# Kernel tuning notes

Hardware: AMD Instinct MI355X
Metric: run time of the kernel (lower is better)

## Reference

```python
import jax, jax.numpy as jnp
import numpy as np

# shapes
B, S, D, V = 2, 2048, 1024, 32000
C = 8            # n_cycles
P = 256          # actual planes = min(n_planes_init, D // 2)
EPS = 1.1920929e-07  # torch RMSNorm default eps for float32 (finfo.eps)


def _rmsnorm(x, w):
    ms = jnp.mean(x * x, axis=-1, keepdims=True)
    return x * jax.lax.rsqrt(ms + EPS) * w


def setup_inputs() -> dict:
    key = jax.random.key(0)
    ks = jax.random.split(key, 10)
    tokens = jax.random.randint(ks[0], (B, S), 0, V, dtype=jnp.int32)
    embed_weight = jax.random.normal(ks[1], (V, D), dtype=jnp.float32) * 0.02
    lm_head_weight = jax.random.normal(ks[2], (V, D), dtype=jnp.float32) * 0.02
    out_norm_weight = jnp.ones((D,), dtype=jnp.float32)
    # per-cycle learned params (non-trivial values for numerics)
    angles = jax.random.normal(ks[3], (C, P), dtype=jnp.float32) * 0.1
    scales = 1.0 + jax.random.normal(ks[4], (C, D), dtype=jnp.float32) * 0.01
    shifts = jax.random.normal(ks[5], (C, D), dtype=jnp.float32) * 0.01
    norm_weights = 1.0 + jax.random.normal(ks[6], (C, D), dtype=jnp.float32) * 0.01
    mix_weight = jnp.array([0.1, 0.8, 0.1], dtype=jnp.float32)
    # plane pairs: per-cycle permutation of D, pi = perm[:P], pj = perm[P:2P]
    pi_list, pj_list = [], []
    for c in range(C):
        perm = jax.random.permutation(jax.random.fold_in(ks[7], c), D)
        pi_list.append(perm[:P])
        pj_list.append(perm[P:2 * P])
    pi_all = jnp.stack(pi_list).astype(jnp.int32)  # [C, P]
    pj_all = jnp.stack(pj_list).astype(jnp.int32)  # [C, P]
    return {
        "tokens": tokens,
        "embed_weight": embed_weight,
        "angles": angles,
        "scales": scales,
        "shifts": shifts,
        "norm_weights": norm_weights,
        "mix_weight": mix_weight,
        "out_norm_weight": out_norm_weight,
        "lm_head_weight": lm_head_weight,
        "pi_all": pi_all,
        "pj_all": pj_all,
    }


def reference(tokens, embed_weight, angles, scales, shifts, norm_weights,
              mix_weight, out_norm_weight, lm_head_weight, pi_all, pj_all):
    x = embed_weight[tokens].astype(jnp.float32)  # [B, S, D]
    n_cycles = angles.shape[0]
    for c in range(n_cycles):
        # temporal mix: shifted-left / self / shifted-right
        left = jnp.pad(x[:, :-1, :], ((0, 0), (1, 0), (0, 0)))
        right = jnp.pad(x[:, 1:, :], ((0, 0), (0, 1), (0, 0)))
        x = mix_weight[0] * left + mix_weight[1] * x + mix_weight[2] * right
        # Givens rotations on disjoint plane pairs (gather -> rotate -> scatter)
        pi, pj = pi_all[c], pj_all[c]
        cos_a = jnp.cos(angles[c])
        sin_a = jnp.sin(angles[c])
        xi = x[..., pi]  # [B, S, P]
        xj = x[..., pj]
        x_new = x.at[..., pi].set(xi * cos_a - xj * sin_a)
        x_new = x_new.at[..., pj].set(xi * sin_a + xj * cos_a)
        # scale/shift + SiLU, then RMSNorm residual update
        x_act = jax.nn.silu(x_new * scales[c] + shifts[c])
        x = x + _rmsnorm(x_act - x, norm_weights[c])
    x = _rmsnorm(x, out_norm_weight)
    return jnp.einsum("bsd,vd->bsv", x, lm_head_weight)  # [B, S, V]
```

## Files before the change

### kernel.cpp

```cpp
#include <hip/hip_runtime.h>

#define B_SZ   2
#define S_LEN  2048
#define D_DIM  1024
#define V_DIM  32000
#define NTOK   (B_SZ * S_LEN)
#define NCYC   8
#define NPLANES 256
#define EPS_F  1.1920929e-07f

typedef float  f32x4  __attribute__((ext_vector_type(4)));
typedef __bf16 bf16x8 __attribute__((ext_vector_type(8)));

__device__ __forceinline__ unsigned short f32_to_bf16(float f) {
    unsigned int u = __builtin_bit_cast(unsigned int, f);
    u += 0x7fffu + ((u >> 16) & 1u);
    return (unsigned short)(u >> 16);
}

__device__ __forceinline__ float block_reduce_sum(float v, float* red) {
    const int tid = threadIdx.x;
    #pragma unroll
    for (int off = 32; off > 0; off >>= 1) v += __shfl_down(v, off, 64);
    if ((tid & 63) == 0) red[tid >> 6] = v;
    __syncthreads();
    return red[0] + red[1] + red[2] + red[3];
}

__global__ __launch_bounds__(256) void k_embed(const int* __restrict__ tokens,
                                               const float* __restrict__ table,
                                               float* __restrict__ x) {
    const int t = blockIdx.x;
    const int tok = tokens[t];
    const float4* src = (const float4*)(table + (size_t)tok * D_DIM);
    float4* dst = (float4*)(x + (size_t)t * D_DIM);
    dst[threadIdx.x] = src[threadIdx.x];
}

__global__ __launch_bounds__(256) void k_cycle(
    const float* __restrict__ xin, float* __restrict__ xout,
    const float* __restrict__ angles, const float* __restrict__ scales,
    const float* __restrict__ shifts, const float* __restrict__ normw,
    const float* __restrict__ mixw, const int* __restrict__ pi,
    const int* __restrict__ pj)
{
    __shared__ float lx[D_DIM];
    __shared__ float red[4];
    const int t = blockIdx.x;
    const int s = t & (S_LEN - 1);
    const int tid = threadIdx.x;
    const int d0 = tid * 4;

    float4 sv = ((const float4*)(xin + (size_t)t * D_DIM))[tid];
    float4 lv = make_float4(0.f, 0.f, 0.f, 0.f);
    float4 rv = make_float4(0.f, 0.f, 0.f, 0.f);
    if (s > 0)         lv = ((const float4*)(xin + (size_t)(t - 1) * D_DIM))[tid];
    if (s < S_LEN - 1) rv = ((const float4*)(xin + (size_t)(t + 1) * D_DIM))[tid];
    const float mw0 = mixw[0], mw1 = mixw[1], mw2 = mixw[2];

    const float m0 = mw0 * lv.x + mw1 * sv.x + mw2 * rv.x;
    const float m1 = mw0 * lv.y + mw1 * sv.y + mw2 * rv.y;
    const float m2 = mw0 * lv.z + mw1 * sv.z + mw2 * rv.z;
    const float m3 = mw0 * lv.w + mw1 * sv.w + mw2 * rv.w;
    lx[d0 + 0] = m0; lx[d0 + 1] = m1; lx[d0 + 2] = m2; lx[d0 + 3] = m3;
    __syncthreads();

    const int ip = pi[tid], jp = pj[tid];
    float sa, ca;
    sincosf(angles[tid], &sa, &ca);
    const float xi = lx[ip], xj = lx[jp];
    __syncthreads();
    lx[ip] = xi * ca - xj * sa;
    lx[jp] = xi * sa + xj * ca;
    __syncthreads();

    const float4 sc = ((const float4*)scales)[tid];
    const float4 sh = ((const float4*)shifts)[tid];
    const float4 nw = ((const float4*)normw)[tid];
    const float xn0 = lx[d0 + 0], xn1 = lx[d0 + 1], xn2 = lx[d0 + 2], xn3 = lx[d0 + 3];
    const float a0 = xn0 * sc.x + sh.x;
    const float a1 = xn1 * sc.y + sh.y;
    const float a2 = xn2 * sc.z + sh.z;
    const float a3 = xn3 * sc.w + sh.w;
    const float r0 = a0 / (1.f + expf(-a0)) - m0;
    const float r1 = a1 / (1.f + expf(-a1)) - m1;
    const float r2 = a2 / (1.f + expf(-a2)) - m2;
    const float r3 = a3 / (1.f + expf(-a3)) - m3;

    const float tot = block_reduce_sum(r0 * r0 + r1 * r1 + r2 * r2 + r3 * r3, red);
    const float inv = rsqrtf(tot * (1.0f / D_DIM) + EPS_F);

    float4 o;
    o.x = m0 + r0 * inv * nw.x;
    o.y = m1 + r1 * inv * nw.y;
    o.z = m2 + r2 * inv * nw.z;
    o.w = m3 + r3 * inv * nw.w;
    ((float4*)(xout + (size_t)t * D_DIM))[tid] = o;
}

__global__ __launch_bounds__(256) void k_final(const float* __restrict__ xin,
                                               const float* __restrict__ ow,
                                               unsigned short* __restrict__ xb)
{
    __shared__ float red[4];
    const int t = blockIdx.x, tid = threadIdx.x;
    const float4 v = ((const float4*)(xin + (size_t)t * D_DIM))[tid];
    const float tot = block_reduce_sum(v.x * v.x + v.y * v.y + v.z * v.z + v.w * v.w, red);
    const float inv = rsqrtf(tot * (1.0f / D_DIM) + EPS_F);
    const float4 w = ((const float4*)ow)[tid];
    ushort4 o = make_ushort4(f32_to_bf16(v.x * inv * w.x),
                             f32_to_bf16(v.y * inv * w.y),
                             f32_to_bf16(v.z * inv * w.z),
                             f32_to_bf16(v.w * inv * w.w));
    ((ushort4*)xb)[(size_t)t * 256 + tid] = o;
}

__global__ __launch_bounds__(256) void k_cvt(const float* __restrict__ w,
                                             unsigned short* __restrict__ wb, int n4)
{
    int i = blockIdx.x * 256 + threadIdx.x;
    const int stride = gridDim.x * 256;
    for (; i < n4; i += stride) {
        const float4 v = ((const float4*)w)[i];
        ushort4 o = make_ushort4(f32_to_bf16(v.x), f32_to_bf16(v.y),
                                 f32_to_bf16(v.z), f32_to_bf16(v.w));
        ((ushort4*)wb)[i] = o;
    }
}

#define GLD_LDS(g, l)                                                          \
    __builtin_amdgcn_global_load_lds(                                          \
        (const __attribute__((address_space(1))) void*)(g),                    \
        (__attribute__((address_space(3))) void*)(l), 16, 0, 0)

#define STAGE_A(BUF, H, KT) do {                                               \
    GLD_LDS(gA + (size_t)(H) * 131072 + (size_t)(KT) * 64,                     \
            &lds[(BUF) * 32768 + (H) * 8192 + wave * 1024]);                   \
    GLD_LDS(gA + (size_t)(H) * 131072 + 8192 + (size_t)(KT) * 64,              \
            &lds[(BUF) * 32768 + (H) * 8192 + wave * 1024 + 512]);             \
} while (0)

#define STAGE_B(BUF, H, KT) do {                                               \
    GLD_LDS(gB + (size_t)(H) * 131072 + (size_t)(KT) * 64,                     \
            &lds[16384 + (BUF) * 32768 + (H) * 8192 + wave * 1024]);           \
    GLD_LDS(gB + (size_t)(H) * 131072 + 8192 + (size_t)(KT) * 64,              \
            &lds[16384 + (BUF) * 32768 + (H) * 8192 + wave * 1024 + 512]);     \
} while (0)

#define RD_A(BUF, MIB) do { _Pragma("unroll")                                  \
    for (int q_ = 0; q_ < 4; ++q_) {                                           \
        afr[q_][0] = *(const bf16x8*)&lds[(BUF) * 32768 + aoff + ((MIB) + q_) * 1024 + kx0]; \
        afr[q_][1] = *(const bf16x8*)&lds[(BUF) * 32768 + aoff + ((MIB) + q_) * 1024 + kx1]; \
    } } while (0)

#define RD_B(BUF, NIB, DST) do { _Pragma("unroll")                             \
    for (int n_ = 0; n_ < 2; ++n_) {                                           \
        DST[n_][0] = *(const bf16x8*)&lds[(BUF) * 32768 + boff + ((NIB) + n_) * 1024 + kx0]; \
        DST[n_][1] = *(const bf16x8*)&lds[(BUF) * 32768 + boff + ((NIB) + n_) * 1024 + kx1]; \
    } } while (0)

#define MFMA16(MIB, NIB, BF) do {                                              \
    __builtin_amdgcn_s_setprio(1);                                             \
    _Pragma("unroll") for (int m_ = 0; m_ < 4; ++m_)                           \
    _Pragma("unroll") for (int n_ = 0; n_ < 2; ++n_) {                         \
        acc[(MIB) + m_][(NIB) + n_] = __builtin_amdgcn_mfma_f32_16x16x32_bf16( \
            afr[m_][0], BF[n_][0], acc[(MIB) + m_][(NIB) + n_], 0, 0, 0);      \
        acc[(MIB) + m_][(NIB) + n_] = __builtin_amdgcn_mfma_f32_16x16x32_bf16( \
            afr[m_][1], BF[n_][1], acc[(MIB) + m_][(NIB) + n_], 0, 0, 0);      \
    }                                                                          \
    __builtin_amdgcn_s_setprio(0); } while (0)

#define PH_SYNC() do { __builtin_amdgcn_s_barrier();                           \
    asm volatile("s_waitcnt lgkmcnt(0)" ::: "memory"); } while (0)
#define PH_END() do { asm volatile("" ::: "memory");                           \
    __builtin_amdgcn_s_barrier(); } while (0)
#define VMCNT4() asm volatile("s_waitcnt vmcnt(4)" ::: "memory")

__global__ __launch_bounds__(512, 2) void k_gemm(
    const unsigned short* __restrict__ A,
    const unsigned short* __restrict__ Bw,
    float* __restrict__ C)
{
    __shared__ __align__(16) unsigned short lds[65536];
    const int tid = threadIdx.x;
    const int wave = tid >> 6, lane = tid & 63;
    const int wm = wave >> 2, wn = wave & 3;
    const int lr = lane & 15, kg = lane >> 4;

    const int swz = (blockIdx.x & 7) * 250 + (blockIdx.x >> 3);
    const int bm = swz / 125, bn = swz % 125;

    const int xr  = (lane & 7) * 8;
    const int kx0 = (kg * 8) ^ xr;
    const int kx1 = (32 + kg * 8) ^ xr;
    const int aoff = (wm * 128 + lr) * 64;
    const int boff = 16384 + (wn * 64 + lr) * 64;

    const int srow = lane >> 3;
    const int scol = ((lane & 7) ^ srow) * 8;
    const unsigned short* gA = A  + (size_t)(bm * 256 + wave * 16 + srow) * 1024 + scol;
    const unsigned short* gB = Bw + (size_t)(bn * 256 + wave * 16 + srow) * 1024 + scol;

    f32x4 acc[8][4];
    #pragma unroll
    for (int i = 0; i < 8; ++i)
        #pragma unroll
        for (int j = 0; j < 4; ++j) acc[i][j] = (f32x4){0.f, 0.f, 0.f, 0.f};
    bf16x8 afr[4][2], b01[2][2], b23[2][2];

    STAGE_A(0, 0, 0); STAGE_A(0, 1, 0);
    STAGE_B(0, 0, 0); STAGE_B(0, 1, 0);
    STAGE_B(1, 0, 1); STAGE_B(1, 1, 1);
    VMCNT4();
    __builtin_amdgcn_s_barrier();

    for (int j = 0; j < 8; ++j) {
        const int k1 = (2 * j + 1) & 15;
        const int k2 = (2 * j + 2) & 15;
        const int k3 = (2 * j + 3) & 15;
        RD_A(0, 0); RD_B(0, 0, b01);
        STAGE_A(1, 0, k1);
        PH_SYNC(); MFMA16(0, 0, b01); PH_END();

        RD_B(0, 2, b23);
        STAGE_A(1, 1, k1);
        PH_SYNC(); MFMA16(0, 2, b23); PH_END();

        RD_A(0, 4);
        STAGE_B(0, 0, k2);
        PH_SYNC(); MFMA16(4, 2, b23); PH_END();

        STAGE_B(0, 1, k2);
        VMCNT4();
        PH_SYNC(); MFMA16(4, 0, b01); PH_END();
        RD_A(1, 0); RD_B(1, 0, b01);
        STAGE_A(0, 0, k2);
        PH_SYNC(); MFMA16(0, 0, b01); PH_END();

        RD_B(1, 2, b23);
        STAGE_A(0, 1, k2);
        PH_SYNC(); MFMA16(0, 2, b23); PH_END();

        RD_A(1, 4);
        STAGE_B(1, 0, k3);
        PH_SYNC(); MFMA16(4, 2, b23); PH_END();

        STAGE_B(1, 1, k3);
        VMCNT4();
        PH_SYNC(); MFMA16(4, 0, b01); PH_END();
    }

    #pragma unroll
    for (int mi = 0; mi < 8; ++mi) {
        const size_t m0 = (size_t)(bm * 256 + wm * 128 + mi * 16 + kg * 4);
        #pragma unroll
        for (int ni = 0; ni < 4; ++ni) {
            const int n = bn * 256 + wn * 64 + ni * 16 + lr;
            float* cp = C + m0 * V_DIM + n;
            cp[0]                 = acc[mi][ni][0];
            cp[(size_t)V_DIM]     = acc[mi][ni][1];
            cp[(size_t)2 * V_DIM] = acc[mi][ni][2];
            cp[(size_t)3 * V_DIM] = acc[mi][ni][3];
        }
    }
}

extern "C" void kernel_launch(void* const* d_in, const int* in_sizes, int n_in,
                              void* d_out, int out_size, void* d_ws, size_t ws_size,
                              hipStream_t stream)
{
    const int*   tokens = (const int*)  d_in[0];
    const float* embedw = (const float*)d_in[1];
    const float* angles = (const float*)d_in[2];
    const float* scales = (const float*)d_in[3];
    const float* shifts = (const float*)d_in[4];
    const float* normw  = (const float*)d_in[5];
    const float* mixw   = (const float*)d_in[6];
    const float* outnw  = (const float*)d_in[7];
    const float* lmhead = (const float*)d_in[8];
    const int*   pi_all = (const int*)  d_in[9];
    const int*   pj_all = (const int*)  d_in[10];
    float* out = (float*)d_out;

    float* xa = (float*)d_ws;
    float* xb = xa + (size_t)NTOK * D_DIM;
    unsigned short* xbf = (unsigned short*)(xb + (size_t)NTOK * D_DIM);
    unsigned short* wbf = xbf + (size_t)NTOK * D_DIM;

    k_embed<<<NTOK, 256, 0, stream>>>(tokens, embedw, xa);

    const float* cin = xa;
    float* cout = xb;
    for (int c = 0; c < NCYC; ++c) {
        k_cycle<<<NTOK, 256, 0, stream>>>(cin, cout,
            angles + c * NPLANES, scales + c * D_DIM, shifts + c * D_DIM,
            normw + c * D_DIM, mixw, pi_all + c * NPLANES, pj_all + c * NPLANES);
        float* tmp = (float*)cin; cin = cout; cout = tmp;
    }

    k_final<<<NTOK, 256, 0, stream>>>(cin, outnw, xbf);
    k_cvt<<<2048, 256, 0, stream>>>(lmhead, wbf, (V_DIM * D_DIM) / 4);
    k_gemm<<<16 * 125, 512, 0, stream>>>(xbf, wbf, out);
}
```

Before: 466.2 us.

## Fuse embed, cycles, final norm and weight conversion into tiled cycle kernels

Merges the embedding gather into the first cycle kernel, the final RMSNorm plus bf16 cast into the last, and spreads the lm_head fp32-to-bf16 conversion across the eight cycle launches. Each block now handles four consecutive tokens, so the neighbour rows needed by the temporal mix are loaded once per group instead of three times per token. The GEMM tile mapping switches from div/mod to shifts with a different block order, and logits are written with nontemporal stores. This removes three launches and redundant global reads, at the cost of more shared memory and registers per block.

```diff
diff --git a/kernel.cpp b/kernel.cpp
--- a/kernel.cpp
+++ b/kernel.cpp
@@ -18,113 +18,161 @@
     return (unsigned short)(u >> 16);
 }
 
-__device__ __forceinline__ float block_reduce_sum(float v, float* red) {
-    const int tid = threadIdx.x;
-    #pragma unroll
-    for (int off = 32; off > 0; off >>= 1) v += __shfl_down(v, off, 64);
-    if ((tid & 63) == 0) red[tid >> 6] = v;
-    __syncthreads();
-    return red[0] + red[1] + red[2] + red[3];
-}
-
-__global__ __launch_bounds__(256) void k_embed(const int* __restrict__ tokens,
-                                               const float* __restrict__ table,
-                                               float* __restrict__ x) {
-    const int t = blockIdx.x;
-    const int tok = tokens[t];
-    const float4* src = (const float4*)(table + (size_t)tok * D_DIM);
-    float4* dst = (float4*)(x + (size_t)t * D_DIM);
-    dst[threadIdx.x] = src[threadIdx.x];
-}
-
-__global__ __launch_bounds__(256) void k_cycle(
+__device__ __forceinline__ float4 mix3(float a, const float4& u, float b,
+                                       const float4& v, float c, const float4& w) {
+    return make_float4(a * u.x + b * v.x + c * w.x,
+                       a * u.y + b * v.y + c * w.y,
+                       a * u.z + b * v.z + c * w.z,
+                       a * u.w + b * v.w + c * w.w);
+}
+
+__global__ __launch_bounds__(256) void k_cyc(
+    int c,
+    const int* __restrict__ tokens, const float* __restrict__ table,
     const float* __restrict__ xin, float* __restrict__ xout,
     const float* __restrict__ angles, const float* __restrict__ scales,
     const float* __restrict__ shifts, const float* __restrict__ normw,
-    const float* __restrict__ mixw, const int* __restrict__ pi,
-    const int* __restrict__ pj)
+    const float* __restrict__ mixw, const float* __restrict__ outnw,
+    unsigned short* __restrict__ xbf,
+    const int* __restrict__ pi, const int* __restrict__ pj,
+    const float* __restrict__ lmhead, unsigned short* __restrict__ wbf)
 {
-    __shared__ float lx[D_DIM];
-    __shared__ float red[4];
-    const int t = blockIdx.x;
-    const int s = t & (S_LEN - 1);
-    const int tid = threadIdx.x;
-    const int d0 = tid * 4;
-
-    float4 sv = ((const float4*)(xin + (size_t)t * D_DIM))[tid];
-    float4 lv = make_float4(0.f, 0.f, 0.f, 0.f);
-    float4 rv = make_float4(0.f, 0.f, 0.f, 0.f);
-    if (s > 0)         lv = ((const float4*)(xin + (size_t)(t - 1) * D_DIM))[tid];
-    if (s < S_LEN - 1) rv = ((const float4*)(xin + (size_t)(t + 1) * D_DIM))[tid];
+    __shared__ float lx[4][D_DIM];
+    __shared__ float red[4][4];
+    const int b = blockIdx.x, tid = threadIdx.x;
+    const int wv = tid >> 6, ln = tid & 63;
+    const int t0 = b << 2;
+    const int s0 = t0 & (S_LEN - 1);
+
+    float4 row[4];
+    float4 hl = make_float4(0.f, 0.f, 0.f, 0.f);
+    float4 hr = make_float4(0.f, 0.f, 0.f, 0.f);
+    if (c == 0) {
+        #pragma unroll
+        for (int i = 0; i < 4; ++i) {
+            const int tok = tokens[t0 + i];
+            row[i] = ((const float4*)(table + (size_t)tok * D_DIM))[tid];
+        }
+        if (s0 > 0) {
+            const int tok = tokens[t0 - 1];
+            hl = ((const float4*)(table + (size_t)tok * D_DIM))[tid];
+        }
+        if (s0 + 4 < S_LEN) {
+            const int tok = tokens[t0 + 4];
+            hr = ((const float4*)(table + (size_t)tok * D_DIM))[tid];
+        }
+    } else {
+        #pragma unroll
+        for (int i = 0; i < 4; ++i)
+            row[i] = ((const float4*)(xin + (size_t)(t0 + i) * D_DIM))[tid];
+        if (s0 > 0)
+            hl = ((const float4*)(xin + (size_t)(t0 - 1) * D_DIM))[tid];
+        if (s0 + 4 < S_LEN)
+            hr = ((const float4*)(xin + (size_t)(t0 + 4) * D_DIM))[tid];
+    }
     const float mw0 = mixw[0], mw1 = mixw[1], mw2 = mixw[2];
 
-    const float m0 = mw0 * lv.x + mw1 * sv.x + mw2 * rv.x;
-    const float m1 = mw0 * lv.y + mw1 * sv.y + mw2 * rv.y;
-    const float m2 = mw0 * lv.z + mw1 * sv.z + mw2 * rv.z;
-    const float m3 = mw0 * lv.w + mw1 * sv.w + mw2 * rv.w;
-    lx[d0 + 0] = m0; lx[d0 + 1] = m1; lx[d0 + 2] = m2; lx[d0 + 3] = m3;
+    float4 m[4];
+    m[0] = mix3(mw0, hl,     mw1, row[0], mw2, row[1]);
+    m[1] = mix3(mw0, row[0], mw1, row[1], mw2, row[2]);
+    m[2] = mix3(mw0, row[1], mw1, row[2], mw2, row[3]);
+    m[3] = mix3(mw0, row[2], mw1, row[3], mw2, hr);
+    #pragma unroll
+    for (int i = 0; i < 4; ++i) ((float4*)lx[i])[tid] = m[i];
     __syncthreads();
 
     const int ip = pi[tid], jp = pj[tid];
     float sa, ca;
     sincosf(angles[tid], &sa, &ca);
-    const float xi = lx[ip], xj = lx[jp];
-    __syncthreads();
-    lx[ip] = xi * ca - xj * sa;
-    lx[jp] = xi * sa + xj * ca;
+    float xi[4], xj[4];
+    #pragma unroll
+    for (int i = 0; i < 4; ++i) { xi[i] = lx[i][ip]; xj[i] = lx[i][jp]; }
+    #pragma unroll
+    for (int i = 0; i < 4; ++i) {
+        lx[i][ip] = xi[i] * ca - xj[i] * sa;
+        lx[i][jp] = xi[i] * sa + xj[i] * ca;
+    }
     __syncthreads();
 
     const float4 sc = ((const float4*)scales)[tid];
     const float4 sh = ((const float4*)shifts)[tid];
     const float4 nw = ((const float4*)normw)[tid];
-    const float xn0 = lx[d0 + 0], xn1 = lx[d0 + 1], xn2 = lx[d0 + 2], xn3 = lx[d0 + 3];
-    const float a0 = xn0 * sc.x + sh.x;
-    const float a1 = xn1 * sc.y + sh.y;
-    const float a2 = xn2 * sc.z + sh.z;
-    const float a3 = xn3 * sc.w + sh.w;
-    const float r0 = a0 / (1.f + expf(-a0)) - m0;
-    const float r1 = a1 / (1.f + expf(-a1)) - m1;
-    const float r2 = a2 / (1.f + expf(-a2)) - m2;
-    const float r3 = a3 / (1.f + expf(-a3)) - m3;
-
-    const float tot = block_reduce_sum(r0 * r0 + r1 * r1 + r2 * r2 + r3 * r3, red);
-    const float inv = rsqrtf(tot * (1.0f / D_DIM) + EPS_F);
-
-    float4 o;
-    o.x = m0 + r0 * inv * nw.x;
-    o.y = m1 + r1 * inv * nw.y;
-    o.z = m2 + r2 * inv * nw.z;
-    o.w = m3 + r3 * inv * nw.w;
-    ((float4*)(xout + (size_t)t * D_DIM))[tid] = o;
-}
-
-__global__ __launch_bounds__(256) void k_final(const float* __restrict__ xin,
-                                               const float* __restrict__ ow,
-                                               unsigned short* __restrict__ xb)
-{
-    __shared__ float red[4];
-    const int t = blockIdx.x, tid = threadIdx.x;
-    const float4 v = ((const float4*)(xin + (size_t)t * D_DIM))[tid];
-    const float tot = block_reduce_sum(v.x * v.x + v.y * v.y + v.z * v.z + v.w * v.w, red);
-    const float inv = rsqrtf(tot * (1.0f / D_DIM) + EPS_F);
-    const float4 w = ((const float4*)ow)[tid];
-    ushort4 o = make_ushort4(f32_to_bf16(v.x * inv * w.x),
-                             f32_to_bf16(v.y * inv * w.y),
-                             f32_to_bf16(v.z * inv * w.z),
-                             f32_to_bf16(v.w * inv * w.w));
-    ((ushort4*)xb)[(size_t)t * 256 + tid] = o;
-}
-
-__global__ __launch_bounds__(256) void k_cvt(const float* __restrict__ w,
-                                             unsigned short* __restrict__ wb, int n4)
-{
-    int i = blockIdx.x * 256 + threadIdx.x;
-    const int stride = gridDim.x * 256;
-    for (; i < n4; i += stride) {
-        const float4 v = ((const float4*)w)[i];
-        ushort4 o = make_ushort4(f32_to_bf16(v.x), f32_to_bf16(v.y),
-                                 f32_to_bf16(v.z), f32_to_bf16(v.w));
-        ((ushort4*)wb)[i] = o;
+    float4 r[4];
+    float sum[4];
+    #pragma unroll
+    for (int i = 0; i < 4; ++i) {
+        const float4 xn = ((const float4*)lx[i])[tid];
+        const float a0 = xn.x * sc.x + sh.x;
+        const float a1 = xn.y * sc.y + sh.y;
+        const float a2 = xn.z * sc.z + sh.z;
+        const float a3 = xn.w * sc.w + sh.w;
+        r[i].x = a0 / (1.f + expf(-a0)) - m[i].x;
+        r[i].y = a1 / (1.f + expf(-a1)) - m[i].y;
+        r[i].z = a2 / (1.f + expf(-a2)) - m[i].z;
+        r[i].w = a3 / (1.f + expf(-a3)) - m[i].w;
+        sum[i] = r[i].x * r[i].x + r[i].y * r[i].y
+               + r[i].z * r[i].z + r[i].w * r[i].w;
+    }
+    #pragma unroll
+    for (int off = 32; off > 0; off >>= 1)
+        #pragma unroll
+        for (int i = 0; i < 4; ++i) sum[i] += __shfl_down(sum[i], off, 64);
+    if (ln == 0) {
+        red[wv][0] = sum[0]; red[wv][1] = sum[1];
+        red[wv][2] = sum[2]; red[wv][3] = sum[3];
+    }
+    __syncthreads();
+    #pragma unroll
+    for (int i = 0; i < 4; ++i) {
+        const float tot = red[0][i] + red[1][i] + red[2][i] + red[3][i];
+        const float inv = rsqrtf(tot * (1.0f / D_DIM) + EPS_F);
+        row[i].x = m[i].x + r[i].x * inv * nw.x;
+        row[i].y = m[i].y + r[i].y * inv * nw.y;
+        row[i].z = m[i].z + r[i].z * inv * nw.z;
+        row[i].w = m[i].w + r[i].w * inv * nw.w;
+    }
+
+    if (c == 7) {
+        __syncthreads();
+        float fs[4];
+        #pragma unroll
+        for (int i = 0; i < 4; ++i)
+            fs[i] = row[i].x * row[i].x + row[i].y * row[i].y
+                  + row[i].z * row[i].z + row[i].w * row[i].w;
+        #pragma unroll
+        for (int off = 32; off > 0; off >>= 1)
+            #pragma unroll
+            for (int i = 0; i < 4; ++i) fs[i] += __shfl_down(fs[i], off, 64);
+        if (ln == 0) {
+            red[wv][0] = fs[0]; red[wv][1] = fs[1];
+            red[wv][2] = fs[2]; red[wv][3] = fs[3];
+        }
+        __syncthreads();
+        const float4 w = ((const float4*)outnw)[tid];
+        #pragma unroll
+        for (int i = 0; i < 4; ++i) {
+            const float tot = red[0][i] + red[1][i] + red[2][i] + red[3][i];
+            const float inv = rsqrtf(tot * (1.0f / D_DIM) + EPS_F);
+            const ushort4 o = make_ushort4(f32_to_bf16(row[i].x * inv * w.x),
+                                           f32_to_bf16(row[i].y * inv * w.y),
+                                           f32_to_bf16(row[i].z * inv * w.z),
+                                           f32_to_bf16(row[i].w * inv * w.w));
+            ((ushort4*)xbf)[(size_t)(t0 + i) * 256 + tid] = o;
+        }
+    } else {
+        #pragma unroll
+        for (int i = 0; i < 4; ++i)
+            ((float4*)(xout + (size_t)(t0 + i) * D_DIM))[tid] = row[i];
+    }
+
+    {
+        const int end = (c + 1) * 1024000;
+        for (int i = c * 1024000 + b * 256 + tid; i < end; i += 262144) {
+            const float4 v = ((const float4*)lmhead)[i];
+            const ushort4 o = make_ushort4(f32_to_bf16(v.x), f32_to_bf16(v.y),
+                                           f32_to_bf16(v.z), f32_to_bf16(v.w));
+            ((ushort4*)wbf)[i] = o;
+        }
     }
 }
 
@@ -188,7 +236,7 @@
     const int lr = lane & 15, kg = lane >> 4;
 
     const int swz = (blockIdx.x & 7) * 250 + (blockIdx.x >> 3);
-    const int bm = swz / 125, bn = swz % 125;
+    const int bm = swz & 15, bn = swz >> 4;
 
     const int xr  = (lane & 7) * 8;
     const int kx0 = (kg * 8) ^ xr;
@@ -218,6 +266,7 @@
         const int k1 = (2 * j + 1) & 15;
         const int k2 = (2 * j + 2) & 15;
         const int k3 = (2 * j + 3) & 15;
+
         RD_A(0, 0); RD_B(0, 0, b01);
         STAGE_A(1, 0, k1);
         PH_SYNC(); MFMA16(0, 0, b01); PH_END();
@@ -233,6 +282,7 @@
         STAGE_B(0, 1, k2);
         VMCNT4();
         PH_SYNC(); MFMA16(4, 0, b01); PH_END();
+
         RD_A(1, 0); RD_B(1, 0, b01);
         STAGE_A(0, 0, k2);
         PH_SYNC(); MFMA16(0, 0, b01); PH_END();
@@ -257,10 +307,10 @@
         for (int ni = 0; ni < 4; ++ni) {
             const int n = bn * 256 + wn * 64 + ni * 16 + lr;
             float* cp = C + m0 * V_DIM + n;
-            cp[0]                 = acc[mi][ni][0];
-            cp[(size_t)V_DIM]     = acc[mi][ni][1];
-            cp[(size_t)2 * V_DIM] = acc[mi][ni][2];
-            cp[(size_t)3 * V_DIM] = acc[mi][ni][3];
+            __builtin_nontemporal_store(acc[mi][ni][0], cp);
+            __builtin_nontemporal_store(acc[mi][ni][1], cp + (size_t)V_DIM);
+            __builtin_nontemporal_store(acc[mi][ni][2], cp + (size_t)2 * V_DIM);
+            __builtin_nontemporal_store(acc[mi][ni][3], cp + (size_t)3 * V_DIM);
         }
     }
 }
@@ -287,18 +337,14 @@
     unsigned short* xbf = (unsigned short*)(xb + (size_t)NTOK * D_DIM);
     unsigned short* wbf = xbf + (size_t)NTOK * D_DIM;
 
-    k_embed<<<NTOK, 256, 0, stream>>>(tokens, embedw, xa);
-
-    const float* cin = xa;
-    float* cout = xb;
     for (int c = 0; c < NCYC; ++c) {
-        k_cycle<<<NTOK, 256, 0, stream>>>(cin, cout,
+        const float* xin = (c & 1) ? xb : xa;
+        float* xout = (c & 1) ? xa : xb;
+        k_cyc<<<NTOK / 4, 256, 0, stream>>>(c, tokens, embedw, xin, xout,
             angles + c * NPLANES, scales + c * D_DIM, shifts + c * D_DIM,
-            normw + c * D_DIM, mixw, pi_all + c * NPLANES, pj_all + c * NPLANES);
-        float* tmp = (float*)cin; cin = cout; cout = tmp;
-    }
-
-    k_final<<<NTOK, 256, 0, stream>>>(cin, outnw, xbf);
-    k_cvt<<<2048, 256, 0, stream>>>(lmhead, wbf, (V_DIM * D_DIM) / 4);
+            normw + c * D_DIM, mixw, outnw, xbf,
+            pi_all + c * NPLANES, pj_all + c * NPLANES, lmhead, wbf);
+    }
+
     k_gemm<<<16 * 125, 512, 0, stream>>>(xbf, wbf, out);
 }
```

Result: faster. 425.8 us (-8.7%).
